# Optimization experiments

Measured on AMD Instinct MI355X. Metric: run time of the kernel, lower is better.

Reference implementation:

```python
import jax, jax.numpy as jnp
import numpy as np

LENGTH = 14
THRESHOLD = 0.6
R = 5


def setup_inputs() -> dict:
    key = jax.random.key(0)
    B = 131072
    heatmap = jax.random.uniform(key, (B, 1, LENGTH, LENGTH), dtype=jnp.float32)
    return {"heatmap": heatmap}


def _nms_masks(heatmap):
    hm = heatmap[:, 0]  # [B,14,14]
    B = hm.shape[0]
    heat = jnp.where(hm > THRESHOLD, hm, 0.0).reshape(B, LENGTH * LENGTH)
    grid = jnp.arange(LENGTH)
    idxs = []
    # 4 rounds of argmax + zero-out-window suppression (fixed small loop)
    for _ in range(4):
        idx = jnp.argmax(heat, axis=1)  # [B]
        x = idx // LENGTH
        y = idx % LENGTH
        x1 = jnp.maximum(x - R, 0)
        y1 = jnp.maximum(y - R, 0)
        x2 = jnp.minimum(x + R, 15)  # original clamps at 15 (exclusive end)
        y2 = jnp.minimum(y + R, 15)
        rowm = (grid[None, :] >= x1[:, None]) & (grid[None, :] < x2[:, None])  # [B,14]
        colm = (grid[None, :] >= y1[:, None]) & (grid[None, :] < y2[:, None])  # [B,14]
        win = (rowm[:, :, None] & colm[:, None, :]).reshape(B, LENGTH * LENGTH)
        heat = jnp.where(win, 0.0, heat)
        idxs.append(idx)
    idxs = jnp.stack(idxs, axis=1)  # [B,4]
    coords = jnp.stack([idxs // LENGTH, idxs % LENGTH], axis=-1)  # [B,4,2]
    # pickTwo: choose the pair (among the 6) with max squared distance
    pairs = jnp.array([[0, 1], [0, 2], [0, 3], [1, 2], [1, 3], [2, 3]])
    pc = coords[:, pairs]  # [B,6,2,2]
    dists = jnp.sum((pc[:, :, 1] - pc[:, :, 0]) ** 2, axis=-1)  # [B,6]
    best = jnp.argmax(dists, axis=1)  # [B] (first max on ties, like np.argmax)
    co = jnp.take_along_axis(pc, best[:, None, None, None], axis=1)[:, 0]  # [B,2,2]
    # Voronoi-style masks: pixel belongs to mask1 iff strictly closer to co1
    u = jnp.arange(LENGTH)[:, None]  # [14,1]
    v = jnp.arange(LENGTH)[None, :]  # [1,14]
    d1 = (u[None] - co[:, 0, 0, None, None]) ** 2 + (v[None] - co[:, 0, 1, None, None]) ** 2
    d2 = (u[None] - co[:, 1, 0, None, None]) ** 2 + (v[None] - co[:, 1, 1, None, None]) ** 2
    m1 = (d1 < d2).astype(jnp.float32)  # [B,14,14]
    m2 = 1.0 - m1  # (m1 < 0.9).float() with m1 in {0,1}
    return m1[:, None], m2[:, None]  # [B,1,14,14] each


def reference(heatmap):
    return _nms_masks(heatmap)
```

## Files before the change

kernel.cpp:

```cpp
#include <hip/hip_runtime.h>


typedef float v4f __attribute__((ext_vector_type(4)));

constexpr int L = 14;
constexpr int NPIX = L * L;
constexpr int NV4 = NPIX / 4;

template <int CTRL>
__device__ __forceinline__ unsigned dpp_maxu(unsigned x) {
    unsigned y = (unsigned)__builtin_amdgcn_update_dpp(0, (int)x, CTRL, 0xF, 0xF, true);
    return x > y ? x : y;
}
__device__ __forceinline__ unsigned row_max16u(unsigned x) {
    x = dpp_maxu<0xB1>(x);
    x = dpp_maxu<0x4E>(x);
    x = dpp_maxu<0x141>(x);
    x = dpp_maxu<0x140>(x);
    return x;
}
__device__ __forceinline__ unsigned umax2(unsigned a, unsigned b) { return a > b ? a : b; }
__device__ __forceinline__ unsigned umax3(unsigned a, unsigned b, unsigned c) {
    return umax2(umax2(a, b), c);
}

__global__ __launch_bounds__(256) void nms_kernel(const v4f* __restrict__ hm4,
                                                  v4f* __restrict__ out4, int B) {
    const int lane = threadIdx.x & 63;
    const int s = lane & 15;
    const int b = blockIdx.x * 16 + ((threadIdx.x >> 6) << 2) + (lane >> 4);
    if (b >= B) return;

    const v4f* __restrict__ bp = hm4 + (size_t)b * NV4;
    v4f a0 = bp[s];
    v4f a1 = bp[16 + s];
    v4f a2 = bp[32 + s];
    v4f a3 = {0.f, 0.f, 0.f, 0.f};
    if (s == 0) a3 = bp[48];

    unsigned key[16];
    int xy[16];
    const int s4 = s << 2;
#pragma unroll
    for (int i = 0; i < 16; ++i) {
        const int fl = s4 + ((i >> 2) << 6) + (i & 3);
        const int x = fl / L, y = fl - (fl / L) * L;
        xy[i] = (x << 8) | y;
        const float v = (i < 4) ? a0[i] : (i < 8) ? a1[i - 4] : (i < 12) ? a2[i - 8] : a3[i - 12];
        const unsigned inv = 255u - (unsigned)fl;
        const unsigned kpos = (((__float_as_uint(v) & 0x7FFFFFu) + 1u) << 8) | inv;
        key[i] = (v > 0.6f) ? kpos : inv;
    }

    int peaks[4];
#pragma unroll
    for (int r = 0; r < 4; ++r) {
        const unsigned t0 = umax3(key[0], key[1], key[2]);
        const unsigned t1 = umax3(key[3], key[4], key[5]);
        const unsigned t2 = umax3(key[6], key[7], key[8]);
        const unsigned t3 = umax3(key[9], key[10], key[11]);
        const unsigned t4 = umax3(key[12], key[13], key[14]);
        unsigned mk = umax2(umax3(t0, t1, t2), umax3(t3, t4, key[15]));
        mk = row_max16u(mk);
        const int flat = 255 - (int)(mk & 255u);
        peaks[r] = flat;
        if (r < 3) {
            const int ax = flat / L;
            const int ay = flat - ax * L;
            const int q = (ax - 5) * 256 + (ay - 5);
#pragma unroll
            for (int i = 0; i < 16; ++i) {
                const int rr = xy[i] - q;
                const bool in = ((rr & 255) < 10) & (((unsigned)rr >> 8) < 10u);
                key[i] = in ? (key[i] & 255u) : key[i];
            }
        }
    }

    int cx[4], cy[4];
#pragma unroll
    for (int i = 0; i < 4; ++i) {
        cx[i] = peaks[i] / L;
        cy[i] = peaks[i] - cx[i] * L;
    }

    const int pa[6] = {0, 0, 0, 1, 1, 2};
    const int pb[6] = {1, 2, 3, 2, 3, 3};
    int bestd = -1, ax0 = 0, ay0 = 0, ax1 = 0, ay1 = 0;
#pragma unroll
    for (int p = 0; p < 6; ++p) {
        const int dx = cx[pb[p]] - cx[pa[p]];
        const int dy = cy[pb[p]] - cy[pa[p]];
        const int d = dx * dx + dy * dy;
        if (d > bestd) { bestd = d; ax0 = cx[pa[p]]; ay0 = cy[pa[p]];
                         ax1 = cx[pb[p]]; ay1 = cy[pb[p]]; }
    }

    const int Ax = (ax1 - ax0) * 2, Ay = (ay1 - ay0) * 2;
    const int K = (ax1 - ax0) * (ax0 + ax1) + (ay1 - ay0) * (ay0 + ay1);

    v4f* __restrict__ o1 = out4 + (size_t)b * NV4;
    v4f* __restrict__ o2 = out4 + (size_t)(B + b) * NV4;
#pragma unroll
    for (int g = 0; g < 4; ++g) {
        v4f mv, nv;
#pragma unroll
        for (int j = 0; j < 4; ++j) {
            const int i = (g << 2) + j;
            const int x = xy[i] >> 8, y = xy[i] & 255;
            const bool t = (Ax * x + Ay * y) < K;
            mv[j] = t ? 1.0f : 0.0f;
            nv[j] = t ? 0.0f : 1.0f;
        }
        if (g < 3) {
            o1[(g << 4) + s] = mv;
            o2[(g << 4) + s] = nv;
        } else if (s == 0) {
            o1[48] = mv;
            o2[48] = nv;
        }
    }
}

extern "C" void kernel_launch(void* const* d_in, const int* in_sizes, int n_in,
                              void* d_out, int out_size, void* d_ws, size_t ws_size,
                              hipStream_t stream) {
    const v4f* hm4 = (const v4f*)d_in[0];
    v4f* out4 = (v4f*)d_out;
    const int B = in_sizes[0] / NPIX;
    const int blocks = (B + 15) / 16;
    nms_kernel<<<blocks, 256, 0, stream>>>(hm4, out4, B);
}
```

Baseline: 278.9 us.

## Process four tiles per block with software-prefetched next-tile loads

Result: slower. 297.8 us (+6.8%).

```diff
diff --git a/kernel.cpp b/kernel.cpp
--- a/kernel.cpp
+++ b/kernel.cpp
@@ -6,6 +6,7 @@
 constexpr int L = 14;
 constexpr int NPIX = L * L;
 constexpr int NV4 = NPIX / 4;
+constexpr int TPB = 4;
 
 template <int CTRL>
 __device__ __forceinline__ unsigned dpp_maxu(unsigned x) {
@@ -28,97 +29,129 @@
                                                   v4f* __restrict__ out4, int B) {
     const int lane = threadIdx.x & 63;
     const int s = lane & 15;
-    const int b = blockIdx.x * 16 + ((threadIdx.x >> 6) << 2) + (lane >> 4);
-    if (b >= B) return;
+    const int grp = ((threadIdx.x >> 6) << 2) + (lane >> 4);
 
-    const v4f* __restrict__ bp = hm4 + (size_t)b * NV4;
-    v4f a0 = bp[s];
-    v4f a1 = bp[16 + s];
-    v4f a2 = bp[32 + s];
-    v4f a3 = {0.f, 0.f, 0.f, 0.f};
-    if (s == 0) a3 = bp[48];
-
-    unsigned key[16];
     int xy[16];
+    unsigned inv[16];
     const int s4 = s << 2;
 #pragma unroll
     for (int i = 0; i < 16; ++i) {
         const int fl = s4 + ((i >> 2) << 6) + (i & 3);
         const int x = fl / L, y = fl - (fl / L) * L;
         xy[i] = (x << 8) | y;
-        const float v = (i < 4) ? a0[i] : (i < 8) ? a1[i - 4] : (i < 12) ? a2[i - 8] : a3[i - 12];
-        const unsigned inv = 255u - (unsigned)fl;
-        const unsigned kpos = (((__float_as_uint(v) & 0x7FFFFFu) + 1u) << 8) | inv;
-        key[i] = (v > 0.6f) ? kpos : inv;
+        inv[i] = 255u - (unsigned)fl;
     }
 
-    int peaks[4];
-#pragma unroll
-    for (int r = 0; r < 4; ++r) {
-        const unsigned t0 = umax3(key[0], key[1], key[2]);
-        const unsigned t1 = umax3(key[3], key[4], key[5]);
-        const unsigned t2 = umax3(key[6], key[7], key[8]);
-        const unsigned t3 = umax3(key[9], key[10], key[11]);
-        const unsigned t4 = umax3(key[12], key[13], key[14]);
-        unsigned mk = umax2(umax3(t0, t1, t2), umax3(t3, t4, key[15]));
-        mk = row_max16u(mk);
-        const int flat = 255 - (int)(mk & 255u);
-        peaks[r] = flat;
-        if (r < 3) {
-            const int ax = flat / L;
-            const int ay = flat - ax * L;
-            const int q = (ax - 5) * 256 + (ay - 5);
-#pragma unroll
-            for (int i = 0; i < 16; ++i) {
-                const int rr = xy[i] - q;
-                const bool in = ((rr & 255) < 10) & (((unsigned)rr >> 8) < 10u);
-                key[i] = in ? (key[i] & 255u) : key[i];
-            }
+    const int tile0 = blockIdx.x * TPB;
+
+    v4f c0, c1, c2, c3 = {0.f, 0.f, 0.f, 0.f};
+    {
+        const int b = tile0 * 16 + grp;
+        if (b < B) {
+            const v4f* __restrict__ bp = hm4 + (size_t)b * NV4;
+            c0 = bp[s];
+            c1 = bp[16 + s];
+            c2 = bp[32 + s];
+            if (s == 0) c3 = bp[48];
         }
     }
 
-    int cx[4], cy[4];
 #pragma unroll
-    for (int i = 0; i < 4; ++i) {
-        cx[i] = peaks[i] / L;
-        cy[i] = peaks[i] - cx[i] * L;
-    }
+    for (int t = 0; t < TPB; ++t) {
+        v4f n0 = {0.f, 0.f, 0.f, 0.f}, n1 = n0, n2 = n0, n3 = n0;
+        if (t + 1 < TPB) {
+            const int bn = (tile0 + t + 1) * 16 + grp;
+            if (bn < B) {
+                const v4f* __restrict__ bp = hm4 + (size_t)bn * NV4;
+                n0 = bp[s];
+                n1 = bp[16 + s];
+                n2 = bp[32 + s];
+                if (s == 0) n3 = bp[48];
+            }
+        }
 
-    const int pa[6] = {0, 0, 0, 1, 1, 2};
-    const int pb[6] = {1, 2, 3, 2, 3, 3};
-    int bestd = -1, ax0 = 0, ay0 = 0, ax1 = 0, ay1 = 0;
+        const int b = (tile0 + t) * 16 + grp;
+        if (b < B) {
+            unsigned key[16];
 #pragma unroll
-    for (int p = 0; p < 6; ++p) {
-        const int dx = cx[pb[p]] - cx[pa[p]];
-        const int dy = cy[pb[p]] - cy[pa[p]];
-        const int d = dx * dx + dy * dy;
-        if (d > bestd) { bestd = d; ax0 = cx[pa[p]]; ay0 = cy[pa[p]];
-                         ax1 = cx[pb[p]]; ay1 = cy[pb[p]]; }
-    }
+            for (int i = 0; i < 16; ++i) {
+                const float v = (i < 4) ? c0[i] : (i < 8) ? c1[i - 4]
+                              : (i < 12) ? c2[i - 8] : c3[i - 12];
+                const unsigned kpos = (((__float_as_uint(v) & 0x7FFFFFu) + 1u) << 8) | inv[i];
+                key[i] = (v > 0.6f) ? kpos : inv[i];
+            }
 
-    const int Ax = (ax1 - ax0) * 2, Ay = (ay1 - ay0) * 2;
-    const int K = (ax1 - ax0) * (ax0 + ax1) + (ay1 - ay0) * (ay0 + ay1);
+            int peaks[4];
+#pragma unroll
+            for (int r = 0; r < 4; ++r) {
+                const unsigned t0 = umax3(key[0], key[1], key[2]);
+                const unsigned t1 = umax3(key[3], key[4], key[5]);
+                const unsigned t2 = umax3(key[6], key[7], key[8]);
+                const unsigned t3 = umax3(key[9], key[10], key[11]);
+                const unsigned t4 = umax3(key[12], key[13], key[14]);
+                unsigned mk = umax2(umax3(t0, t1, t2), umax3(t3, t4, key[15]));
+                mk = row_max16u(mk);
+                const int flat = 255 - (int)(mk & 255u);
+                peaks[r] = flat;
+                if (r < 3) {
+                    const int ax = flat / L;
+                    const int ay = flat - ax * L;
+                    const int q = (ax - 5) * 256 + (ay - 5);
+#pragma unroll
+                    for (int i = 0; i < 16; ++i) {
+                        const int rr = xy[i] - q;
+                        const bool in = ((rr & 255) < 10) & (((unsigned)rr >> 8) < 10u);
+                        key[i] = in ? (key[i] & 255u) : key[i];
+                    }
+                }
+            }
 
-    v4f* __restrict__ o1 = out4 + (size_t)b * NV4;
-    v4f* __restrict__ o2 = out4 + (size_t)(B + b) * NV4;
+            int cx[4], cy[4];
 #pragma unroll
-    for (int g = 0; g < 4; ++g) {
-        v4f mv, nv;
+            for (int i = 0; i < 4; ++i) {
+                cx[i] = peaks[i] / L;
+                cy[i] = peaks[i] - cx[i] * L;
+            }
+
+            const int pa[6] = {0, 0, 0, 1, 1, 2};
+            const int pb[6] = {1, 2, 3, 2, 3, 3};
+            int bestd = -1, ax0 = 0, ay0 = 0, ax1 = 0, ay1 = 0;
 #pragma unroll
-        for (int j = 0; j < 4; ++j) {
-            const int i = (g << 2) + j;
-            const int x = xy[i] >> 8, y = xy[i] & 255;
-            const bool t = (Ax * x + Ay * y) < K;
-            mv[j] = t ? 1.0f : 0.0f;
-            nv[j] = t ? 0.0f : 1.0f;
+            for (int p = 0; p < 6; ++p) {
+                const int dx = cx[pb[p]] - cx[pa[p]];
+                const int dy = cy[pb[p]] - cy[pa[p]];
+                const int d = dx * dx + dy * dy;
+                if (d > bestd) { bestd = d; ax0 = cx[pa[p]]; ay0 = cy[pa[p]];
+                                 ax1 = cx[pb[p]]; ay1 = cy[pb[p]]; }
+            }
+
+            const int Ax = (ax1 - ax0) * 2, Ay = (ay1 - ay0) * 2;
+            const int K = (ax1 - ax0) * (ax0 + ax1) + (ay1 - ay0) * (ay0 + ay1);
+
+            v4f* __restrict__ o1 = out4 + (size_t)b * NV4;
+            v4f* __restrict__ o2 = out4 + (size_t)(B + b) * NV4;
+#pragma unroll
+            for (int g = 0; g < 4; ++g) {
+                v4f mv, nv;
+#pragma unroll
+                for (int j = 0; j < 4; ++j) {
+                    const int i = (g << 2) + j;
+                    const int x = xy[i] >> 8, y = xy[i] & 255;
+                    const bool tt = (Ax * x + Ay * y) < K;
+                    mv[j] = tt ? 1.0f : 0.0f;
+                    nv[j] = tt ? 0.0f : 1.0f;
+                }
+                if (g < 3) {
+                    o1[(g << 4) + s] = mv;
+                    o2[(g << 4) + s] = nv;
+                } else if (s == 0) {
+                    o1[48] = mv;
+                    o2[48] = nv;
+                }
+            }
         }
-        if (g < 3) {
-            o1[(g << 4) + s] = mv;
-            o2[(g << 4) + s] = nv;
-        } else if (s == 0) {
-            o1[48] = mv;
-            o2[48] = nv;
-        }
+
+        c0 = n0; c1 = n1; c2 = n2; c3 = n3;
     }
 }
 
@@ -128,6 +161,7 @@
     const v4f* hm4 = (const v4f*)d_in[0];
     v4f* out4 = (v4f*)d_out;
     const int B = in_sizes[0] / NPIX;
-    const int blocks = (B + 15) / 16;
+    const int ntiles = (B + 15) / 16;
+    const int blocks = (ntiles + TPB - 1) / TPB;
     nms_kernel<<<blocks, 256, 0, stream>>>(hm4, out4, B);
 }
```
